# Performance work log

Measured on AMD Instinct MI355X. Metric: run time of the kernel, lower is better.

Reference implementation:

```python
import jax, jax.numpy as jnp
import numpy as np

NUM_HEADS = 16
DIM = 1024
HD = DIM // NUM_HEADS  # 64


def setup_inputs() -> dict:
    key = jax.random.key(0)
    ks = jax.random.split(key, 7)
    B, S = 4, 2048
    def xavier(k, shape, fan_in, fan_out):
        bound = float(np.sqrt(6.0 / (fan_in + fan_out)))
        return jax.random.uniform(k, shape, jnp.float32, -bound, bound)
    return {
        "q": jax.random.normal(ks[0], (B, S, DIM), jnp.float32),
        "k": jax.random.normal(ks[1], (B, S, DIM), jnp.float32),
        "v": jax.random.normal(ks[2], (B, S, DIM), jnp.float32),
        "Wq": xavier(ks[3], (NUM_HEADS, DIM, HD), DIM, HD),
        "Wk": xavier(ks[4], (NUM_HEADS, DIM, HD), DIM, HD),
        "Wv": xavier(ks[5], (NUM_HEADS, DIM, HD), DIM, HD),
        "Wo": xavier(ks[6], (DIM, DIM), DIM, DIM),
    }


def reference(q, k, v, Wq, Wk, Wv, Wo):
    B, S, D = q.shape
    norm = jnp.sqrt(jnp.asarray(HD, q.dtype))
    # per-head projections: [B,S,D] x [H,D,hd] -> [B,H,S,hd]
    qh = jnp.einsum('bsd,hde->bhse', q, Wq)
    kh = jnp.einsum('bsd,hde->bhse', k, Wk)
    vh = jnp.einsum('bsd,hde->bhse', v, Wv)
    # scores [B,H,S,S]
    scores = jnp.einsum('bhse,bhte->bhst', qh, kh) / norm
    causal = jnp.triu(jnp.ones((S, S), bool), k=1)
    scores = jnp.where(causal, -jnp.inf, scores)
    attn = jax.nn.softmax(scores, axis=-1)
    out = jnp.einsum('bhst,bhte->bhse', attn, vh)  # [B,H,S,hd]
    # faithful to original: a raw view of [B,H,S,hd] -> [B,S,H*hd] (no head transpose)
    out = out.reshape(B, S, NUM_HEADS * HD)
    return jnp.matmul(out, Wo)
```

## Files before the change

### kernel.cpp

```cpp
#include <hip/hip_runtime.h>
#include <hip/hip_bf16.h>
#include <stdint.h>

typedef __bf16 bf16;
typedef __bf16 bf16x8 __attribute__((ext_vector_type(8)));
typedef __bf16 bf16x4 __attribute__((ext_vector_type(4)));
typedef __bf16 bf16x2 __attribute__((ext_vector_type(2)));
typedef float f32x4 __attribute__((ext_vector_type(4)));
typedef float f32x16 __attribute__((ext_vector_type(16)));
typedef int i32x4 __attribute__((ext_vector_type(4)));

#define NH   16
#define SEQ  2048
#define DM   1024
#define HD   64

__device__ __forceinline__ int swz(int r, int o) {
  return o ^ ((r & 7) << 4) ^ (((r >> 3) & 1) << 5);
}

__device__ __forceinline__ int tauK(int m) {
  return (m & ~12) | ((m & 4) << 1) | ((m & 8) >> 1);
}

__device__ __forceinline__ void gll16(const void* g, void* l) {
  __builtin_amdgcn_global_load_lds(
      (__attribute__((address_space(1))) unsigned int*)(g),
      (__attribute__((address_space(3))) unsigned int*)(l), 16, 0, 0);
}

__device__ __forceinline__ int pk2(float a, float b) {
  bf16x2 t; t[0] = (bf16)a; t[1] = (bf16)b;
  return __builtin_bit_cast(int, t);
}

__global__ __launch_bounds__(256) void conv_wt(const float* __restrict__ Wq,
                                               const float* __restrict__ Wk,
                                               const float* __restrict__ Wv,
                                               const float* __restrict__ Wo,
                                               bf16* __restrict__ WqT,
                                               bf16* __restrict__ WkT,
                                               bf16* __restrict__ WvT,
                                               bf16* __restrict__ WoT) {
  __shared__ float tile[64][65];
  int z = blockIdx.z, t = threadIdx.x;
  int d0 = blockIdx.x << 6;
  if (z < 3) {
    const float* W = (z == 0 ? Wq : z == 1 ? Wk : Wv) + ((size_t)blockIdx.y << 16);
#pragma unroll
    for (int i = 0; i < 4; ++i) {
      int slot = (i << 8) + t;
      int r = slot >> 4, c4 = (slot & 15) << 2;
      float4 fv = *(const float4*)(W + (size_t)(d0 + r) * 64 + c4);
      tile[r][c4] = fv.x; tile[r][c4 + 1] = fv.y;
      tile[r][c4 + 2] = fv.z; tile[r][c4 + 3] = fv.w;
    }
  } else {
    int n0 = blockIdx.y << 6;
#pragma unroll
    for (int i = 0; i < 4; ++i) {
      int slot = (i << 8) + t;
      int r = slot >> 4, c4 = (slot & 15) << 2;
      float4 fv = *(const float4*)(Wo + (size_t)(d0 + r) * 1024 + n0 + c4);
      tile[r][c4] = fv.x; tile[r][c4 + 1] = fv.y;
      tile[r][c4 + 2] = fv.z; tile[r][c4 + 3] = fv.w;
    }
  }
  __syncthreads();
  bf16* Wt = z == 0 ? WqT : z == 1 ? WkT : z == 2 ? WvT : WoT;
  size_t base = (z < 3) ? ((size_t)blockIdx.y << 16)
                        : (size_t)(blockIdx.y << 6) * 1024;
  int e = t >> 2, dq = (t & 3) << 4;
  bf16x8 o0, o1;
#pragma unroll
  for (int j = 0; j < 8; ++j) {
    o0[j] = (bf16)tile[dq + j][e];
    o1[j] = (bf16)tile[dq + 8 + j][e];
  }
  bf16* p = Wt + base + (size_t)e * 1024 + d0 + dq;
  *(bf16x8*)p = o0;
  *(bf16x8*)(p + 8) = o1;
}

__global__ __launch_bounds__(256) void conv_in(const float* __restrict__ q,
                                               const float* __restrict__ k,
                                               const float* __restrict__ v,
                                               bf16* __restrict__ qb,
                                               bf16* __restrict__ kb,
                                               bf16* __restrict__ vb) {
  int z = blockIdx.y;
  const float* src = z == 0 ? q : z == 1 ? k : v;
  bf16* dst = z == 0 ? qb : z == 1 ? kb : vb;
  int i = (blockIdx.x * 256 + threadIdx.x) << 4;
  float4 f0 = *(const float4*)(src + i);
  float4 f1 = *(const float4*)(src + i + 4);
  float4 f2 = *(const float4*)(src + i + 8);
  float4 f3 = *(const float4*)(src + i + 12);
  bf16x8 o0, o1;
  o0[0] = (bf16)f0.x; o0[1] = (bf16)f0.y; o0[2] = (bf16)f0.z; o0[3] = (bf16)f0.w;
  o0[4] = (bf16)f1.x; o0[5] = (bf16)f1.y; o0[6] = (bf16)f1.z; o0[7] = (bf16)f1.w;
  o1[0] = (bf16)f2.x; o1[1] = (bf16)f2.y; o1[2] = (bf16)f2.z; o1[3] = (bf16)f2.w;
  o1[4] = (bf16)f3.x; o1[5] = (bf16)f3.y; o1[6] = (bf16)f3.z; o1[7] = (bf16)f3.w;
  *(bf16x8*)(dst + i) = o0;
  *(bf16x8*)(dst + i + 8) = o1;
}

template <bool AF32>
__device__ __forceinline__ void gemm_body(char* sm, const void* Av,
                                          const bf16* Bt, void* Cv, int epi,
                                          float scale, int n0, int m0) {
  char* As = sm;
  char* Bs = sm + 16384;
  int tid = threadIdx.x;
  int wid = tid >> 6, lane = tid & 63;
  int g = lane >> 4, cc = lane & 15;
  int wr = wid >> 1, wc = wid & 1;

  f32x4 acc[4][4];
#pragma unroll
  for (int a = 0; a < 4; ++a)
#pragma unroll
    for (int b = 0; b < 4; ++b)
#pragma unroll
      for (int j = 0; j < 4; ++j) acc[a][b][j] = 0.0f;

  for (int kt = 0; kt < 16; ++kt) {
    int k0 = kt << 6;
#pragma unroll
    for (int it = 0; it < 4; ++it) {
      int L = (it << 12) + (tid << 4);
      int r = L >> 7, o = L & 127;
      int os = swz(r, o);
      gll16(Bt + (size_t)(n0 + r) * 1024 + k0 + (os >> 1),
            Bs + (it << 12) + (wid << 10));
    }
    if constexpr (AF32) {
      const float* A = (const float*)Av;
      int r = tid >> 1, hf = tid & 1;
      const float* src = A + (size_t)(m0 + r) * 1024 + k0 + hf * 32;
      float4 fv[8];
#pragma unroll
      for (int q = 0; q < 8; ++q) fv[q] = ((const float4*)src)[q];
#pragma unroll
      for (int q = 0; q < 4; ++q) {
        float4 a = fv[2 * q], b = fv[2 * q + 1];
        bf16x8 pk;
        pk[0] = (bf16)a.x; pk[1] = (bf16)a.y; pk[2] = (bf16)a.z; pk[3] = (bf16)a.w;
        pk[4] = (bf16)b.x; pk[5] = (bf16)b.y; pk[6] = (bf16)b.z; pk[7] = (bf16)b.w;
        *(bf16x8*)(As + (r << 7) + swz(r, hf * 64 + q * 16)) = pk;
      }
    } else {
      const bf16* A = (const bf16*)Av;
#pragma unroll
      for (int it = 0; it < 4; ++it) {
        int L = (it << 12) + (tid << 4);
        int r = L >> 7, o = L & 127;
        int os = swz(r, o);
        gll16(A + (size_t)(m0 + r) * 1024 + k0 + (os >> 1),
              As + (it << 12) + (wid << 10));
      }
    }
    __syncthreads();
#pragma unroll
    for (int kk = 0; kk < 2; ++kk) {
      bf16x8 af[4], bfr[4];
#pragma unroll
      for (int fm = 0; fm < 4; ++fm) {
        int r = (wr << 6) + (fm << 4) + cc;
        af[fm] = *(const bf16x8*)(As + (r << 7) + swz(r, (kk << 6) + (g << 4)));
      }
#pragma unroll
      for (int fn = 0; fn < 4; ++fn) {
        int r = (wc << 6) + (fn << 4) + cc;
        bfr[fn] = *(const bf16x8*)(Bs + (r << 7) + swz(r, (kk << 6) + (g << 4)));
      }
#pragma unroll
      for (int fm = 0; fm < 4; ++fm)
#pragma unroll
        for (int fn = 0; fn < 4; ++fn)
          acc[fm][fn] = __builtin_amdgcn_mfma_f32_16x16x32_bf16(
              af[fm], bfr[fn], acc[fm][fn], 0, 0, 0);
    }
    __syncthreads();
  }

#pragma unroll
  for (int fm = 0; fm < 4; ++fm) {
#pragma unroll
    for (int fn = 0; fn < 4; ++fn) {
      f32x4 v = acc[fm][fn];
      int mr = m0 + (wr << 6) + (fm << 4) + (g << 2);
      int n = n0 + (wc << 6) + (fn << 4) + cc;
      if (epi == 2) {
        float* C = (float*)Cv;
#pragma unroll
        for (int j = 0; j < 4; ++j) C[(size_t)(mr + j) * 1024 + n] = v[j];
      } else if (epi == 0) {
        bf16* C = (bf16*)Cv;
        int h = n >> 6, e = n & 63;
#pragma unroll
        for (int j = 0; j < 4; ++j) {
          int b = (mr + j) >> 11, s = (mr + j) & 2047;
          C[((size_t)(b * NH + h) * SEQ + s) * HD + e] = (bf16)(v[j] * scale);
        }
      } else {
        bf16* C = (bf16*)Cv;
        int h = n >> 6, e = n & 63;
        int b = mr >> 11, s = mr & 2047;
        bf16x4 t;
#pragma unroll
        for (int j = 0; j < 4; ++j) t[j] = (bf16)v[j];
        *(bf16x4*)(C + ((size_t)(b * NH + h) * HD + e) * SEQ + s) = t;
      }
    }
  }
}

__global__ __launch_bounds__(256, 4) void gemm_qkv_bf16(
    const bf16* __restrict__ qb, const bf16* __restrict__ kb,
    const bf16* __restrict__ vb, const bf16* __restrict__ Wq,
    const bf16* __restrict__ Wk, const bf16* __restrict__ Wv,
    bf16* __restrict__ Qh, bf16* __restrict__ Kh, bf16* __restrict__ Vt,
    float qscale) {
  __shared__ char sm[32768];
  int z = (int)blockIdx.y >> 3;
  int nt = (int)blockIdx.y & 7;
  const void* A = z == 0 ? (const void*)qb : z == 1 ? (const void*)kb : (const void*)vb;
  const bf16* B = z == 0 ? Wq : z == 1 ? Wk : Wv;
  void* C = z == 0 ? (void*)Qh : z == 1 ? (void*)Kh : (void*)Vt;
  gemm_body<false>(sm, A, B, C, z == 2 ? 1 : 0, z == 0 ? qscale : 1.0f,
                   nt << 7, (int)blockIdx.x << 7);
}

__global__ __launch_bounds__(256, 2) void gemm_qkv_f32(
    const float* __restrict__ q, const float* __restrict__ k,
    const float* __restrict__ v, const bf16* __restrict__ Wq,
    const bf16* __restrict__ Wk, const bf16* __restrict__ Wv,
    bf16* __restrict__ Qh, bf16* __restrict__ Kh, bf16* __restrict__ Vt,
    float qscale) {
  __shared__ char sm[32768];
  int z = blockIdx.z;
  const void* A = z == 0 ? (const void*)q : z == 1 ? (const void*)k : (const void*)v;
  const bf16* B = z == 0 ? Wq : z == 1 ? Wk : Wv;
  void* C = z == 0 ? (void*)Qh : z == 1 ? (void*)Kh : (void*)Vt;
  gemm_body<true>(sm, A, B, C, z == 2 ? 1 : 0, z == 0 ? qscale : 1.0f,
                  (int)blockIdx.x << 7, (int)blockIdx.y << 7);
}

__global__ __launch_bounds__(256, 4) void gemm_o(const bf16* __restrict__ Att,
                                                 const bf16* __restrict__ Wo,
                                                 float* __restrict__ out) {
  __shared__ char sm[32768];
  gemm_body<false>(sm, Att, Wo, out, 2, 1.0f,
                   (int)blockIdx.y << 7, (int)blockIdx.x << 7);
}

__global__ __launch_bounds__(128, 2) void attn_fwd(const bf16* __restrict__ Qh,
                                                   const bf16* __restrict__ Kh,
                                                   const bf16* __restrict__ Vt,
                                                   bf16* __restrict__ Oa) {
  __shared__ char sm[32768];
  int tid = threadIdx.x, wid = tid >> 6;
  int lane = tid & 63, cc = lane & 31, hi = lane >> 5;
  int bx = blockIdx.x, by = blockIdx.y;
  int bh = (bx << 3) + (by >> 4);
  int pr = by & 15;
  const bf16* Kb = Kh + (size_t)bh * SEQ * HD;
  const bf16* Vb = Vt + (size_t)bh * HD * SEQ;

  bf16x8 vones;
#pragma unroll
  for (int j = 0; j < 8; ++j) vones[j] = (bf16)1.0f;

  for (int ph = 0; ph < 2; ++ph) {
    int qx = ph ? (31 - pr) : pr;
    int q0 = qx << 6;
    int sb = q0 + (wid << 5);

    const bf16* Qp = Qh + ((size_t)bh * SEQ + sb + cc) * HD + (hi << 3);
    bf16x8 qf[4];
#pragma unroll
    for (int kk = 0; kk < 4; ++kk) qf[kk] = *(const bf16x8*)(Qp + (kk << 4));

    f32x16 acc[2], lac;
#pragma unroll
    for (int eb = 0; eb < 2; ++eb)
#pragma unroll
      for (int r = 0; r < 16; ++r) acc[eb][r] = 0.f;
#pragma unroll
    for (int r = 0; r < 16; ++r) lac[r] = 0.f;

    int nkv = qx + 1;
    int cur = 0;
#pragma unroll
    for (int i2 = 0; i2 < 4; ++i2) {
      int L = (i2 << 11) + (tid << 4);
      int r = L >> 7, o = L & 127;
      int os = swz(r, o);
      gll16(Kb + (size_t)tauK(r) * HD + (os >> 1),
            sm + (i2 << 11) + (wid << 10));
      gll16(Vb + (size_t)r * SEQ + (os >> 1),
            sm + 8192 + (i2 << 11) + (wid << 10));
    }
    asm volatile("s_waitcnt vmcnt(0)" ::: "memory");
    __builtin_amdgcn_s_barrier();
    __builtin_amdgcn_sched_barrier(0);

    for (int it = 0; it < nkv; ++it) {
      int t0 = it << 6;
      char* Ks = sm + (cur << 14);
      char* Vs = Ks + 8192;
      if (it + 1 < nkv) {
        char* nb = sm + ((cur ^ 1) << 14);
        int t1 = t0 + 64;
#pragma unroll
        for (int i2 = 0; i2 < 4; ++i2) {
          int L = (i2 << 11) + (tid << 4);
          int r = L >> 7, o = L & 127;
          int os = swz(r, o);
          gll16(Kb + (size_t)(t1 + tauK(r)) * HD + (os >> 1),
                nb + (i2 << 11) + (wid << 10));
          gll16(Vb + (size_t)r * SEQ + t1 + (os >> 1),
                nb + 8192 + (i2 << 11) + (wid << 10));
        }
      }
      if (t0 <= sb + 31) {
        f32x16 sc[2];
#pragma unroll
        for (int tb = 0; tb < 2; ++tb) {
#pragma unroll
          for (int r = 0; r < 16; ++r) sc[tb][r] = 0.f;
#pragma unroll
          for (int kk = 0; kk < 4; ++kk) {
            int rr = (tb << 5) + cc;
            bf16x8 kf = *(const bf16x8*)(Ks + (rr << 7) +
                                         swz(rr, (kk << 5) + (hi << 4)));
            sc[tb] = __builtin_amdgcn_mfma_f32_32x32x16_bf16(kf, qf[kk],
                                                             sc[tb], 0, 0, 0);
          }
        }
        if (t0 + 63 > sb) {
          int s = sb + cc;
#pragma unroll
          for (int tb = 0; tb < 2; ++tb)
#pragma unroll
            for (int r = 0; r < 16; ++r) {
              int t = t0 + (tb << 5) + (r & 3) + (((r >> 2) & 1) << 2) +
                      (hi << 3) + ((r >> 3) << 4);
              if (t > s) sc[tb][r] = -3e38f;
            }
        }
#pragma unroll
        for (int tb = 0; tb < 2; ++tb)
#pragma unroll
          for (int r = 0; r < 16; ++r) sc[tb][r] = exp2f(sc[tb][r]);
#pragma unroll
        for (int ks = 0; ks < 4; ++ks) {
          int tb = ks >> 1, base = (ks & 1) << 3;
          i32x4 wv;
          wv[0] = pk2(sc[tb][base + 0], sc[tb][base + 1]);
          wv[1] = pk2(sc[tb][base + 2], sc[tb][base + 3]);
          wv[2] = pk2(sc[tb][base + 4], sc[tb][base + 5]);
          wv[3] = pk2(sc[tb][base + 6], sc[tb][base + 7]);
          bf16x8 pa = __builtin_bit_cast(bf16x8, wv);
          lac = __builtin_amdgcn_mfma_f32_32x32x16_bf16(pa, vones, lac,
                                                        0, 0, 0);
#pragma unroll
          for (int eb = 0; eb < 2; ++eb) {
            int rr = (eb << 5) + cc;
            bf16x8 vf = *(const bf16x8*)(Vs + (rr << 7) +
                                         swz(rr, (ks << 5) + (hi << 4)));
            acc[eb] = __builtin_amdgcn_mfma_f32_32x32x16_bf16(pa, vf,
                                                              acc[eb], 0, 0, 0);
          }
        }
      }
      asm volatile("s_waitcnt vmcnt(0)" ::: "memory");
      __builtin_amdgcn_s_barrier();
      __builtin_amdgcn_sched_barrier(0);
      cur ^= 1;
    }
    bf16* Op = Oa + ((size_t)bh * SEQ + sb) * HD;
#pragma unroll
    for (int r = 0; r < 16; ++r) {
      float ir = __builtin_amdgcn_rcpf(lac[r]);
      int ssel = (r & 3) + ((r >> 2) << 3) + (hi << 2);
#pragma unroll
      for (int eb = 0; eb < 2; ++eb)
        Op[(size_t)ssel * HD + (eb << 5) + cc] = (bf16)(acc[eb][r] * ir);
    }
  }
}

extern "C" void kernel_launch(void* const* d_in, const int* in_sizes, int n_in,
                              void* d_out, int out_size, void* d_ws,
                              size_t ws_size, hipStream_t stream) {
  const float* q = (const float*)d_in[0];
  const float* k = (const float*)d_in[1];
  const float* v = (const float*)d_in[2];
  const float* Wq = (const float*)d_in[3];
  const float* Wk = (const float*)d_in[4];
  const float* Wv = (const float*)d_in[5];
  const float* Wo = (const float*)d_in[6];
  char* ws = (char*)d_ws;

  const size_t MB = 1024 * 1024;
  const float qscale = 0.125f * 1.44269504f;

  bf16* WqT = (bf16*)(ws + 0 * MB);
  bf16* WkT = (bf16*)(ws + 2 * MB);
  bf16* WvT = (bf16*)(ws + 4 * MB);
  bf16* WoT = (bf16*)(ws + 6 * MB);

  conv_wt<<<dim3(16, 16, 4), 256, 0, stream>>>(Wq, Wk, Wv, Wo,
                                               WqT, WkT, WvT, WoT);

  if (ws_size >= 104 * MB) {
    bf16* qb = (bf16*)(ws + 8 * MB);
    bf16* kb = (bf16*)(ws + 24 * MB);
    bf16* vb = (bf16*)(ws + 40 * MB);
    bf16* Qh = (bf16*)(ws + 56 * MB);
    bf16* Kh = (bf16*)(ws + 72 * MB);
    bf16* Vt = (bf16*)(ws + 88 * MB);
    bf16* Att = qb;

    conv_in<<<dim3(2048, 3), 256, 0, stream>>>(q, k, v, qb, kb, vb);
    gemm_qkv_bf16<<<dim3(64, 24), 256, 0, stream>>>(
        qb, kb, vb, WqT, WkT, WvT, Qh, Kh, Vt, qscale);
    attn_fwd<<<dim3(8, 128), 128, 0, stream>>>(Qh, Kh, Vt, Att);
    gemm_o<<<dim3(64, 8), 256, 0, stream>>>(Att, WoT, (float*)d_out);
  } else {
    bf16* Qh = (bf16*)(ws + 8 * MB);
    bf16* Kh = (bf16*)(ws + 24 * MB);
    bf16* Vt = (bf16*)(ws + 40 * MB);
    bf16* Att = (bf16*)(ws + 56 * MB);

    gemm_qkv_f32<<<dim3(8, 64, 3), 256, 0, stream>>>(
        q, k, v, WqT, WkT, WvT, Qh, Kh, Vt, qscale);
    attn_fwd<<<dim3(8, 128), 128, 0, stream>>>(Qh, Kh, Vt, Att);
    gemm_o<<<dim3(8, 64), 256, 0, stream>>>(Att, WoT, (float*)d_out);
  }
}
```

Baseline: 184.4 us.

## Process two 64-row query tiles per warp to reuse K/V tiles

Each attention block now covers 128 query rows instead of 64, with each warp holding two query fragments that share every K and V tile loaded into LDS. This halves the grid and the number of K/V tile loads per query row, and the final diagonal tile is peeled so only the second query group handles it. The cost is roughly doubled accumulator registers per warp, which may lower occupancy, and half as many blocks to balance the causal load across CUs.

```diff
diff --git a/kernel.cpp b/kernel.cpp
--- a/kernel.cpp
+++ b/kernel.cpp
@@ -263,8 +263,8 @@
   int tid = threadIdx.x, wid = tid >> 6;
   int lane = tid & 63, cc = lane & 31, hi = lane >> 5;
   int bx = blockIdx.x, by = blockIdx.y;
-  int bh = (bx << 3) + (by >> 4);
-  int pr = by & 15;
+  int bh = (bx << 3) + (by >> 3);
+  int pr = by & 7;
   const bf16* Kb = Kh + (size_t)bh * SEQ * HD;
   const bf16* Vb = Vt + (size_t)bh * HD * SEQ;
 
@@ -273,24 +273,29 @@
   for (int j = 0; j < 8; ++j) vones[j] = (bf16)1.0f;
 
   for (int ph = 0; ph < 2; ++ph) {
-    int qx = ph ? (31 - pr) : pr;
-    int q0 = qx << 6;
-    int sb = q0 + (wid << 5);
-
-    const bf16* Qp = Qh + ((size_t)bh * SEQ + sb + cc) * HD + (hi << 3);
-    bf16x8 qf[4];
-#pragma unroll
-    for (int kk = 0; kk < 4; ++kk) qf[kk] = *(const bf16x8*)(Qp + (kk << 4));
-
-    f32x16 acc[2], lac;
+    int qx = ph ? (15 - pr) : pr;
+    int q0 = qx << 7;
+    int sb0 = q0 + (wid << 5);
+    int sb1 = q0 + 64 + (wid << 5);
+
+    const bf16* Qp0 = Qh + ((size_t)bh * SEQ + sb0 + cc) * HD + (hi << 3);
+    const bf16* Qp1 = Qh + ((size_t)bh * SEQ + sb1 + cc) * HD + (hi << 3);
+    bf16x8 qf0[4], qf1[4];
+#pragma unroll
+    for (int kk = 0; kk < 4; ++kk) {
+      qf0[kk] = *(const bf16x8*)(Qp0 + (kk << 4));
+      qf1[kk] = *(const bf16x8*)(Qp1 + (kk << 4));
+    }
+
+    f32x16 acc0[2], acc1[2], lac0, lac1;
 #pragma unroll
     for (int eb = 0; eb < 2; ++eb)
 #pragma unroll
-      for (int r = 0; r < 16; ++r) acc[eb][r] = 0.f;
-#pragma unroll
-    for (int r = 0; r < 16; ++r) lac[r] = 0.f;
-
-    int nkv = qx + 1;
+      for (int r = 0; r < 16; ++r) { acc0[eb][r] = 0.f; acc1[eb][r] = 0.f; }
+#pragma unroll
+    for (int r = 0; r < 16; ++r) { lac0[r] = 0.f; lac1[r] = 0.f; }
+
+    int nkv = (qx << 1) + 2;
     int cur = 0;
 #pragma unroll
     for (int i2 = 0; i2 < 4; ++i2) {
@@ -306,11 +311,11 @@
     __builtin_amdgcn_s_barrier();
     __builtin_amdgcn_sched_barrier(0);
 
-    for (int it = 0; it < nkv; ++it) {
+    for (int it = 0; it < nkv - 1; ++it) {
       int t0 = it << 6;
       char* Ks = sm + (cur << 14);
       char* Vs = Ks + 8192;
-      if (it + 1 < nkv) {
+      {
         char* nb = sm + ((cur ^ 1) << 14);
         int t1 = t0 + 64;
 #pragma unroll
@@ -324,55 +329,65 @@
                 nb + 8192 + (i2 << 11) + (wid << 10));
         }
       }
-      if (t0 <= sb + 31) {
-        f32x16 sc[2];
-#pragma unroll
-        for (int tb = 0; tb < 2; ++tb) {
-#pragma unroll
-          for (int r = 0; r < 16; ++r) sc[tb][r] = 0.f;
-#pragma unroll
-          for (int kk = 0; kk < 4; ++kk) {
-            int rr = (tb << 5) + cc;
-            bf16x8 kf = *(const bf16x8*)(Ks + (rr << 7) +
-                                         swz(rr, (kk << 5) + (hi << 4)));
-            sc[tb] = __builtin_amdgcn_mfma_f32_32x32x16_bf16(kf, qf[kk],
-                                                             sc[tb], 0, 0, 0);
+      f32x16 sc0[2], sc1[2];
+#pragma unroll
+      for (int tb = 0; tb < 2; ++tb) {
+#pragma unroll
+        for (int r = 0; r < 16; ++r) { sc0[tb][r] = 0.f; sc1[tb][r] = 0.f; }
+#pragma unroll
+        for (int kk = 0; kk < 4; ++kk) {
+          int rr = (tb << 5) + cc;
+          bf16x8 kf = *(const bf16x8*)(Ks + (rr << 7) +
+                                       swz(rr, (kk << 5) + (hi << 4)));
+          sc0[tb] = __builtin_amdgcn_mfma_f32_32x32x16_bf16(kf, qf0[kk],
+                                                            sc0[tb], 0, 0, 0);
+          sc1[tb] = __builtin_amdgcn_mfma_f32_32x32x16_bf16(kf, qf1[kk],
+                                                            sc1[tb], 0, 0, 0);
+        }
+      }
+      if (t0 + 63 > sb0) {
+        int s = sb0 + cc;
+#pragma unroll
+        for (int tb = 0; tb < 2; ++tb)
+#pragma unroll
+          for (int r = 0; r < 16; ++r) {
+            int t = t0 + (tb << 5) + (r & 3) + (((r >> 2) & 1) << 2) +
+                    (hi << 3) + ((r >> 3) << 4);
+            if (t > s) sc0[tb][r] = -3e38f;
           }
-        }
-        if (t0 + 63 > sb) {
-          int s = sb + cc;
-#pragma unroll
-          for (int tb = 0; tb < 2; ++tb)
-#pragma unroll
-            for (int r = 0; r < 16; ++r) {
-              int t = t0 + (tb << 5) + (r & 3) + (((r >> 2) & 1) << 2) +
-                      (hi << 3) + ((r >> 3) << 4);
-              if (t > s) sc[tb][r] = -3e38f;
-            }
-        }
-#pragma unroll
-        for (int tb = 0; tb < 2; ++tb)
-#pragma unroll
-          for (int r = 0; r < 16; ++r) sc[tb][r] = exp2f(sc[tb][r]);
-#pragma unroll
-        for (int ks = 0; ks < 4; ++ks) {
-          int tb = ks >> 1, base = (ks & 1) << 3;
-          i32x4 wv;
-          wv[0] = pk2(sc[tb][base + 0], sc[tb][base + 1]);
-          wv[1] = pk2(sc[tb][base + 2], sc[tb][base + 3]);
-          wv[2] = pk2(sc[tb][base + 4], sc[tb][base + 5]);
-          wv[3] = pk2(sc[tb][base + 6], sc[tb][base + 7]);
-          bf16x8 pa = __builtin_bit_cast(bf16x8, wv);
-          lac = __builtin_amdgcn_mfma_f32_32x32x16_bf16(pa, vones, lac,
-                                                        0, 0, 0);
-#pragma unroll
-          for (int eb = 0; eb < 2; ++eb) {
-            int rr = (eb << 5) + cc;
-            bf16x8 vf = *(const bf16x8*)(Vs + (rr << 7) +
-                                         swz(rr, (ks << 5) + (hi << 4)));
-            acc[eb] = __builtin_amdgcn_mfma_f32_32x32x16_bf16(pa, vf,
-                                                              acc[eb], 0, 0, 0);
-          }
+      }
+#pragma unroll
+      for (int tb = 0; tb < 2; ++tb)
+#pragma unroll
+        for (int r = 0; r < 16; ++r) {
+          sc0[tb][r] = exp2f(sc0[tb][r]);
+          sc1[tb][r] = exp2f(sc1[tb][r]);
+        }
+#pragma unroll
+      for (int ks = 0; ks < 4; ++ks) {
+        int tb = ks >> 1, base = (ks & 1) << 3;
+        i32x4 w0, w1;
+        w0[0] = pk2(sc0[tb][base + 0], sc0[tb][base + 1]);
+        w0[1] = pk2(sc0[tb][base + 2], sc0[tb][base + 3]);
+        w0[2] = pk2(sc0[tb][base + 4], sc0[tb][base + 5]);
+        w0[3] = pk2(sc0[tb][base + 6], sc0[tb][base + 7]);
+        w1[0] = pk2(sc1[tb][base + 0], sc1[tb][base + 1]);
+        w1[1] = pk2(sc1[tb][base + 2], sc1[tb][base + 3]);
+        w1[2] = pk2(sc1[tb][base + 4], sc1[tb][base + 5]);
+        w1[3] = pk2(sc1[tb][base + 6], sc1[tb][base + 7]);
+        bf16x8 pa0 = __builtin_bit_cast(bf16x8, w0);
+        bf16x8 pa1 = __builtin_bit_cast(bf16x8, w1);
+        lac0 = __builtin_amdgcn_mfma_f32_32x32x16_bf16(pa0, vones, lac0, 0, 0, 0);
+        lac1 = __builtin_amdgcn_mfma_f32_32x32x16_bf16(pa1, vones, lac1, 0, 0, 0);
+#pragma unroll
+        for (int eb = 0; eb < 2; ++eb) {
+          int rr = (eb << 5) + cc;
+          bf16x8 vf = *(const bf16x8*)(Vs + (rr << 7) +
+                                       swz(rr, (ks << 5) + (hi << 4)));
+          acc0[eb] = __builtin_amdgcn_mfma_f32_32x32x16_bf16(pa0, vf,
+                                                             acc0[eb], 0, 0, 0);
+          acc1[eb] = __builtin_amdgcn_mfma_f32_32x32x16_bf16(pa1, vf,
+                                                             acc1[eb], 0, 0, 0);
         }
       }
       asm volatile("s_waitcnt vmcnt(0)" ::: "memory");
@@ -380,14 +395,66 @@
       __builtin_amdgcn_sched_barrier(0);
       cur ^= 1;
     }
-    bf16* Op = Oa + ((size_t)bh * SEQ + sb) * HD;
+    {
+      int t0 = (nkv - 1) << 6;
+      char* Ks = sm + (cur << 14);
+      char* Vs = Ks + 8192;
+      f32x16 sc1[2];
+#pragma unroll
+      for (int tb = 0; tb < 2; ++tb) {
+#pragma unroll
+        for (int r = 0; r < 16; ++r) sc1[tb][r] = 0.f;
+#pragma unroll
+        for (int kk = 0; kk < 4; ++kk) {
+          int rr = (tb << 5) + cc;
+          bf16x8 kf = *(const bf16x8*)(Ks + (rr << 7) +
+                                       swz(rr, (kk << 5) + (hi << 4)));
+          sc1[tb] = __builtin_amdgcn_mfma_f32_32x32x16_bf16(kf, qf1[kk],
+                                                            sc1[tb], 0, 0, 0);
+        }
+      }
+      int s = sb1 + cc;
+#pragma unroll
+      for (int tb = 0; tb < 2; ++tb)
+#pragma unroll
+        for (int r = 0; r < 16; ++r) {
+          int t = t0 + (tb << 5) + (r & 3) + (((r >> 2) & 1) << 2) +
+                  (hi << 3) + ((r >> 3) << 4);
+          sc1[tb][r] = (t > s) ? 0.f : exp2f(sc1[tb][r]);
+        }
+#pragma unroll
+      for (int ks = 0; ks < 4; ++ks) {
+        int tb = ks >> 1, base = (ks & 1) << 3;
+        i32x4 w1;
+        w1[0] = pk2(sc1[tb][base + 0], sc1[tb][base + 1]);
+        w1[1] = pk2(sc1[tb][base + 2], sc1[tb][base + 3]);
+        w1[2] = pk2(sc1[tb][base + 4], sc1[tb][base + 5]);
+        w1[3] = pk2(sc1[tb][base + 6], sc1[tb][base + 7]);
+        bf16x8 pa1 = __builtin_bit_cast(bf16x8, w1);
+        lac1 = __builtin_amdgcn_mfma_f32_32x32x16_bf16(pa1, vones, lac1, 0, 0, 0);
+#pragma unroll
+        for (int eb = 0; eb < 2; ++eb) {
+          int rr = (eb << 5) + cc;
+          bf16x8 vf = *(const bf16x8*)(Vs + (rr << 7) +
+                                       swz(rr, (ks << 5) + (hi << 4)));
+          acc1[eb] = __builtin_amdgcn_mfma_f32_32x32x16_bf16(pa1, vf,
+                                                             acc1[eb], 0, 0, 0);
+        }
+      }
+      __builtin_amdgcn_s_barrier();
+    }
+    bf16* Op0 = Oa + ((size_t)bh * SEQ + sb0) * HD;
+    bf16* Op1 = Oa + ((size_t)bh * SEQ + sb1) * HD;
 #pragma unroll
     for (int r = 0; r < 16; ++r) {
-      float ir = __builtin_amdgcn_rcpf(lac[r]);
       int ssel = (r & 3) + ((r >> 2) << 3) + (hi << 2);
-#pragma unroll
-      for (int eb = 0; eb < 2; ++eb)
-        Op[(size_t)ssel * HD + (eb << 5) + cc] = (bf16)(acc[eb][r] * ir);
+      float ir0 = __builtin_amdgcn_rcpf(lac0[r]);
+      float ir1 = __builtin_amdgcn_rcpf(lac1[r]);
+#pragma unroll
+      for (int eb = 0; eb < 2; ++eb) {
+        Op0[(size_t)ssel * HD + (eb << 5) + cc] = (bf16)(acc0[eb][r] * ir0);
+        Op1[(size_t)ssel * HD + (eb << 5) + cc] = (bf16)(acc1[eb][r] * ir1);
+      }
     }
   }
 }
@@ -427,7 +494,7 @@
     conv_in<<<dim3(2048, 3), 256, 0, stream>>>(q, k, v, qb, kb, vb);
     gemm_qkv_bf16<<<dim3(64, 24), 256, 0, stream>>>(
         qb, kb, vb, WqT, WkT, WvT, Qh, Kh, Vt, qscale);
-    attn_fwd<<<dim3(8, 128), 128, 0, stream>>>(Qh, Kh, Vt, Att);
+    attn_fwd<<<dim3(8, 64), 128, 0, stream>>>(Qh, Kh, Vt, Att);
     gemm_o<<<dim3(64, 8), 256, 0, stream>>>(Att, WoT, (float*)d_out);
   } else {
     bf16* Qh = (bf16*)(ws + 8 * MB);
@@ -437,7 +504,7 @@
 
     gemm_qkv_f32<<<dim3(8, 64, 3), 256, 0, stream>>>(
         q, k, v, WqT, WkT, WvT, Qh, Kh, Vt, qscale);
-    attn_fwd<<<dim3(8, 128), 128, 0, stream>>>(Qh, Kh, Vt, Att);
+    attn_fwd<<<dim3(8, 64), 128, 0, stream>>>(Qh, Kh, Vt, Att);
     gemm_o<<<dim3(8, 64), 256, 0, stream>>>(Att, WoT, (float*)d_out);
   }
 }
```

Result: slower. 219.2 us (+18.9%).

## Software-pipeline attention loop with triple-buffered K and overlapped QK/PV

Applied to the files above, without the earlier changes.

Restructures the attention inner loop so the QK^T MFMAs for the next KV tile are issued while exp2 and PV run on the current tile. K moves to a triple buffer and V to a double buffer, so loads are prefetched further ahead. The causal mask is applied only on the last tile, and s_setprio wraps the MFMA phases. This is meant to hide exp latency and memory latency behind matrix work, at the cost of more registers (two score sets) and more LDS (40 KB), which may cut occupancy.

```diff
diff --git a/kernel.cpp b/kernel.cpp
--- a/kernel.cpp
+++ b/kernel.cpp
@@ -255,11 +255,103 @@
                    (int)blockIdx.y << 7, (int)blockIdx.x << 7);
 }
 
+__device__ __forceinline__ void stage_k(const bf16* Kb, char* dst, int t0,
+                                        int tid) {
+#pragma unroll
+  for (int i2 = 0; i2 < 4; ++i2) {
+    int L = (i2 << 11) + (tid << 4);
+    int r = L >> 7, o = L & 127;
+    int os = swz(r, o);
+    gll16(Kb + (size_t)(t0 + tauK(r)) * HD + (os >> 1),
+          dst + (i2 << 11) + ((tid >> 6) << 10));
+  }
+}
+__device__ __forceinline__ void stage_v(const bf16* Vb, char* dst, int t0,
+                                        int tid) {
+#pragma unroll
+  for (int i2 = 0; i2 < 4; ++i2) {
+    int L = (i2 << 11) + (tid << 4);
+    int r = L >> 7, o = L & 127;
+    int os = swz(r, o);
+    gll16(Vb + (size_t)r * SEQ + t0 + (os >> 1),
+          dst + (i2 << 11) + ((tid >> 6) << 10));
+  }
+}
+
+#define QK_INTO(SC, KS)                                                     \
+  _Pragma("unroll") for (int tb = 0; tb < 2; ++tb) {                        \
+    _Pragma("unroll") for (int r = 0; r < 16; ++r) SC[tb][r] = 0.f;         \
+    _Pragma("unroll") for (int kk = 0; kk < 4; ++kk) {                      \
+      int rr = (tb << 5) + cc;                                              \
+      bf16x8 kf = *(const bf16x8*)((KS) + (rr << 7) +                       \
+                                   swz(rr, (kk << 5) + (hi << 4)));         \
+      SC[tb] = __builtin_amdgcn_mfma_f32_32x32x16_bf16(kf, qf[kk], SC[tb],  \
+                                                       0, 0, 0);            \
+    }                                                                       \
+  }
+
+#define PV_FROM(SC, VS)                                                     \
+  _Pragma("unroll") for (int ks = 0; ks < 4; ++ks) {                        \
+    int tb = ks >> 1, base = (ks & 1) << 3;                                 \
+    i32x4 wv;                                                               \
+    wv[0] = pk2(SC[tb][base + 0], SC[tb][base + 1]);                        \
+    wv[1] = pk2(SC[tb][base + 2], SC[tb][base + 3]);                        \
+    wv[2] = pk2(SC[tb][base + 4], SC[tb][base + 5]);                        \
+    wv[3] = pk2(SC[tb][base + 6], SC[tb][base + 7]);                        \
+    bf16x8 pa = __builtin_bit_cast(bf16x8, wv);                             \
+    lac = __builtin_amdgcn_mfma_f32_32x32x16_bf16(pa, vones, lac, 0, 0, 0); \
+    _Pragma("unroll") for (int eb = 0; eb < 2; ++eb) {                      \
+      int rr = (eb << 5) + cc;                                              \
+      bf16x8 vf = *(const bf16x8*)((VS) + (rr << 7) +                       \
+                                   swz(rr, (ks << 5) + (hi << 4)));         \
+      acc[eb] = __builtin_amdgcn_mfma_f32_32x32x16_bf16(pa, vf, acc[eb],    \
+                                                        0, 0, 0);           \
+    }                                                                       \
+  }
+
+#define PIPE_BODY(SCC, SCN, IT)                                             \
+  do {                                                                      \
+    char* Kn = sm + (((IT) + 1) % 3) * 8192;                                \
+    char* Vs = sm + 24576 + (((IT) & 1) << 13);                             \
+    __builtin_amdgcn_s_setprio(1);                                          \
+    QK_INTO(SCN, Kn);                                                       \
+    __builtin_amdgcn_s_setprio(0);                                          \
+    _Pragma("unroll") for (int tb = 0; tb < 2; ++tb)                        \
+    _Pragma("unroll") for (int r = 0; r < 16; ++r)                          \
+        SCC[tb][r] = exp2f(SCC[tb][r]);                                     \
+    __builtin_amdgcn_s_setprio(1);                                          \
+    PV_FROM(SCC, Vs);                                                       \
+    __builtin_amdgcn_s_setprio(0);                                          \
+    asm volatile("s_waitcnt vmcnt(0)" ::: "memory");                        \
+    __builtin_amdgcn_s_barrier();                                           \
+    __builtin_amdgcn_sched_barrier(0);                                      \
+    if ((IT) + 3 < nkv)                                                     \
+      stage_k(Kb, sm + ((IT) % 3) * 8192, ((IT) + 3) << 6, tid);            \
+    if ((IT) + 2 < nkv)                                                     \
+      stage_v(Vb, sm + 24576 + (((IT) & 1) << 13), ((IT) + 2) << 6, tid);   \
+  } while (0)
+
+#define TAIL_BODY(SCC)                                                      \
+  do {                                                                      \
+    int t0 = (nkv - 1) << 6;                                                \
+    char* Vs = sm + 24576 + (((nkv - 1) & 1) << 13);                        \
+    int s = sb + cc;                                                        \
+    _Pragma("unroll") for (int tb = 0; tb < 2; ++tb)                        \
+    _Pragma("unroll") for (int r = 0; r < 16; ++r) {                        \
+      int t = t0 + (tb << 5) + (r & 3) + (((r >> 2) & 1) << 2) +            \
+              (hi << 3) + ((r >> 3) << 4);                                  \
+      SCC[tb][r] = (t > s) ? 0.f : exp2f(SCC[tb][r]);                       \
+    }                                                                       \
+    __builtin_amdgcn_s_setprio(1);                                          \
+    PV_FROM(SCC, Vs);                                                       \
+    __builtin_amdgcn_s_setprio(0);                                          \
+  } while (0)
+
 __global__ __launch_bounds__(128, 2) void attn_fwd(const bf16* __restrict__ Qh,
                                                    const bf16* __restrict__ Kh,
                                                    const bf16* __restrict__ Vt,
                                                    bf16* __restrict__ Oa) {
-  __shared__ char sm[32768];
+  __shared__ char sm[40960];
   int tid = threadIdx.x, wid = tid >> 6;
   int lane = tid & 63, cc = lane & 31, hi = lane >> 5;
   int bx = blockIdx.x, by = blockIdx.y;
@@ -291,95 +383,33 @@
     for (int r = 0; r < 16; ++r) lac[r] = 0.f;
 
     int nkv = qx + 1;
-    int cur = 0;
-#pragma unroll
-    for (int i2 = 0; i2 < 4; ++i2) {
-      int L = (i2 << 11) + (tid << 4);
-      int r = L >> 7, o = L & 127;
-      int os = swz(r, o);
-      gll16(Kb + (size_t)tauK(r) * HD + (os >> 1),
-            sm + (i2 << 11) + (wid << 10));
-      gll16(Vb + (size_t)r * SEQ + (os >> 1),
-            sm + 8192 + (i2 << 11) + (wid << 10));
-    }
+
+    stage_k(Kb, sm, 0, tid);
+    stage_v(Vb, sm + 24576, 0, tid);
+    if (nkv > 1) stage_k(Kb, sm + 8192, 64, tid);
     asm volatile("s_waitcnt vmcnt(0)" ::: "memory");
     __builtin_amdgcn_s_barrier();
     __builtin_amdgcn_sched_barrier(0);
-
-    for (int it = 0; it < nkv; ++it) {
-      int t0 = it << 6;
-      char* Ks = sm + (cur << 14);
-      char* Vs = Ks + 8192;
-      if (it + 1 < nkv) {
-        char* nb = sm + ((cur ^ 1) << 14);
-        int t1 = t0 + 64;
-#pragma unroll
-        for (int i2 = 0; i2 < 4; ++i2) {
-          int L = (i2 << 11) + (tid << 4);
-          int r = L >> 7, o = L & 127;
-          int os = swz(r, o);
-          gll16(Kb + (size_t)(t1 + tauK(r)) * HD + (os >> 1),
-                nb + (i2 << 11) + (wid << 10));
-          gll16(Vb + (size_t)r * SEQ + t1 + (os >> 1),
-                nb + 8192 + (i2 << 11) + (wid << 10));
-        }
-      }
-      if (t0 <= sb + 31) {
-        f32x16 sc[2];
-#pragma unroll
-        for (int tb = 0; tb < 2; ++tb) {
-#pragma unroll
-          for (int r = 0; r < 16; ++r) sc[tb][r] = 0.f;
-#pragma unroll
-          for (int kk = 0; kk < 4; ++kk) {
-            int rr = (tb << 5) + cc;
-            bf16x8 kf = *(const bf16x8*)(Ks + (rr << 7) +
-                                         swz(rr, (kk << 5) + (hi << 4)));
-            sc[tb] = __builtin_amdgcn_mfma_f32_32x32x16_bf16(kf, qf[kk],
-                                                             sc[tb], 0, 0, 0);
-          }
-        }
-        if (t0 + 63 > sb) {
-          int s = sb + cc;
-#pragma unroll
-          for (int tb = 0; tb < 2; ++tb)
-#pragma unroll
-            for (int r = 0; r < 16; ++r) {
-              int t = t0 + (tb << 5) + (r & 3) + (((r >> 2) & 1) << 2) +
-                      (hi << 3) + ((r >> 3) << 4);
-              if (t > s) sc[tb][r] = -3e38f;
-            }
-        }
-#pragma unroll
-        for (int tb = 0; tb < 2; ++tb)
-#pragma unroll
-          for (int r = 0; r < 16; ++r) sc[tb][r] = exp2f(sc[tb][r]);
-#pragma unroll
-        for (int ks = 0; ks < 4; ++ks) {
-          int tb = ks >> 1, base = (ks & 1) << 3;
-          i32x4 wv;
-          wv[0] = pk2(sc[tb][base + 0], sc[tb][base + 1]);
-          wv[1] = pk2(sc[tb][base + 2], sc[tb][base + 3]);
-          wv[2] = pk2(sc[tb][base + 4], sc[tb][base + 5]);
-          wv[3] = pk2(sc[tb][base + 6], sc[tb][base + 7]);
-          bf16x8 pa = __builtin_bit_cast(bf16x8, wv);
-          lac = __builtin_amdgcn_mfma_f32_32x32x16_bf16(pa, vones, lac,
-                                                        0, 0, 0);
-#pragma unroll
-          for (int eb = 0; eb < 2; ++eb) {
-            int rr = (eb << 5) + cc;
-            bf16x8 vf = *(const bf16x8*)(Vs + (rr << 7) +
-                                         swz(rr, (ks << 5) + (hi << 4)));
-            acc[eb] = __builtin_amdgcn_mfma_f32_32x32x16_bf16(pa, vf,
-                                                              acc[eb], 0, 0, 0);
-          }
-        }
-      }
-      asm volatile("s_waitcnt vmcnt(0)" ::: "memory");
-      __builtin_amdgcn_s_barrier();
-      __builtin_amdgcn_sched_barrier(0);
-      cur ^= 1;
-    }
+    if (nkv > 2) stage_k(Kb, sm + 16384, 128, tid);
+    if (nkv > 1) stage_v(Vb, sm + 24576 + 8192, 64, tid);
+
+    f32x16 scA[2], scB[2];
+    QK_INTO(scA, sm);
+
+    for (int it = 0; it + 1 < nkv; ++it) {
+      if ((it & 1) == 0) {
+        PIPE_BODY(scA, scB, it);
+      } else {
+        PIPE_BODY(scB, scA, it);
+      }
+    }
+    if (((nkv - 1) & 1) == 0) {
+      TAIL_BODY(scA);
+    } else {
+      TAIL_BODY(scB);
+    }
+    __builtin_amdgcn_s_barrier();
+
     bf16* Op = Oa + ((size_t)bh * SEQ + sb) * HD;
 #pragma unroll
     for (int r = 0; r < 16; ++r) {
```

New measurement: 399.6 us. +116.7%, slower.
